# Kernel tuning notes

Hardware: AMD Instinct MI355X
Metric: run time of the kernel (lower is better)

Reference implementation:

```python
import jax, jax.numpy as jnp
import numpy as np

B, S, LQ = 32, 1024, 128
EMB = 256; H = 256; NH = 8; DH = H // NH
NCATE, NCONT, NNODE = 4, 8, 4
VOCAB = 50000
EPS = 1e-5
LK = S - LQ


def _ln(x, g, b):
    mu = jnp.mean(x, -1, keepdims=True)
    xc = x - mu
    var = jnp.mean(xc * xc, -1, keepdims=True)
    return xc * jax.lax.rsqrt(var + EPS) * g + b


def _leaky(x):
    return jnp.where(x >= 0, x, 0.01 * x)  # LeakyReLU slope 0.01 (torch default)


def setup_inputs() -> dict:
    key = jax.random.key(0)
    ks = jax.random.split(key, 48)
    rnd = lambda i, shape, scale=0.02: jax.random.normal(ks[i], shape, dtype=jnp.float32) * scale
    rng = np.random.default_rng(0)
    qidx = jnp.asarray(np.sort(rng.choice(S, LQ, replace=False)).astype(np.int64))
    cate_table = rnd(6, (VOCAB, EMB)).at[0].set(0.0)  # padding_idx=0
    inp = {
        "node": jax.random.normal(ks[0], (B, S, EMB * NNODE), dtype=jnp.float32),
        "cate": jax.random.randint(ks[1], (B, S, NCATE), 0, VOCAB),
        "cont": jax.random.normal(ks[2], (B, S, NCONT), dtype=jnp.float32),
        "query_index": qidx,
        "mask": jax.random.bernoulli(ks[3], 0.1, (B, LK)),
        "cate_table": cate_table,
        "pos_emb": rnd(4, (1, S, H)),
        "node_W": rnd(5, (EMB * NNODE, H)), "node_b": jnp.zeros((H,), jnp.float32),
        "node_ln_g": jnp.ones((H,), jnp.float32), "node_ln_b": jnp.zeros((H,), jnp.float32),
        "cate_W": rnd(7, (EMB * NCATE, H)), "cate_b": jnp.zeros((H,), jnp.float32),
        "cate_ln_g": jnp.ones((H,), jnp.float32), "cate_ln_b": jnp.zeros((H,), jnp.float32),
        "bn_g": jnp.ones((NCONT,), jnp.float32), "bn_b": jnp.zeros((NCONT,), jnp.float32),
        "cont_W": rnd(8, (NCONT, H)), "cont_b": jnp.zeros((H,), jnp.float32),
        "cont_ln_g": jnp.ones((H,), jnp.float32), "cont_ln_b": jnp.zeros((H,), jnp.float32),
        "comb_W": rnd(9, (3 * H, H)), "comb_b": jnp.zeros((H,), jnp.float32),
        "comb_ln_g": jnp.ones((H,), jnp.float32), "comb_ln_b": jnp.zeros((H,), jnp.float32),
        "q_W": rnd(10, (H, H)), "q_b": jnp.zeros((H,), jnp.float32),
        "k_W": rnd(11, (H, H)), "k_b": jnp.zeros((H,), jnp.float32),
        "v_W": rnd(12, (H, H)), "v_b": jnp.zeros((H,), jnp.float32),
        "reg_W1": rnd(13, (H, H)), "reg_b1": jnp.zeros((H,), jnp.float32),
        "reg_ln_g": jnp.ones((H,), jnp.float32), "reg_ln_b": jnp.zeros((H,), jnp.float32),
        "reg_W2": rnd(14, (H, H)), "reg_b2": jnp.zeros((H,), jnp.float32),
    }
    return inp


def reference(node, cate, cont, query_index, mask, cate_table, pos_emb,
              node_W, node_b, node_ln_g, node_ln_b,
              cate_W, cate_b, cate_ln_g, cate_ln_b,
              bn_g, bn_b, cont_W, cont_b, cont_ln_g, cont_ln_b,
              comb_W, comb_b, comb_ln_g, comb_ln_b,
              q_W, q_b, k_W, k_b, v_W, v_b,
              reg_W1, reg_b1, reg_ln_g, reg_ln_b, reg_W2, reg_b2):
    # --- three embedding branches: Linear -> LayerNorm ---
    node_e = _ln(node @ node_W + node_b, node_ln_g, node_ln_b)
    ce = cate_table[cate].reshape(B, S, NCATE * EMB)  # embedding gather
    cate_e = _ln(ce @ cate_W + cate_b, cate_ln_g, cate_ln_b)
    # BatchNorm1d (training-mode batch stats, biased var) over flattened [B*S, C]
    cf = cont.reshape(-1, NCONT)
    mu = jnp.mean(cf, 0)
    var = jnp.mean((cf - mu) ** 2, 0)
    cn = ((cf - mu) * jax.lax.rsqrt(var + EPS) * bn_g + bn_b).reshape(B, S, NCONT)
    cont_e = _ln(cn @ cont_W + cont_b, cont_ln_g, cont_ln_b)
    # --- combine + positions ---
    seq = jnp.concatenate([node_e, cate_e, cont_e], -1)       # [B,S,3H]
    seq = _ln(_leaky(seq) @ comb_W + comb_b, comb_ln_g, comb_ln_b) + pos_emb  # [B,S,H]
    # --- gather-split cross attention: queries vs complement keys ---
    is_q = jnp.zeros((S,), bool).at[query_index].set(True)
    key_index = jnp.nonzero(~is_q, size=LK)[0]                # setdiff1d, static size
    q = seq[:, query_index]                                   # [B,LQ,H]
    kv = seq[:, key_index]                                    # [B,LK,H]
    Q = (q @ q_W + q_b).reshape(B, LQ, NH, DH).transpose(0, 2, 1, 3)
    K = (kv @ k_W + k_b).reshape(B, LK, NH, DH).transpose(0, 2, 1, 3)
    V = (kv @ v_W + v_b).reshape(B, LK, NH, DH).transpose(0, 2, 1, 3)
    scale = jnp.float32(1.0 / np.sqrt(DH))
    scores = jnp.einsum('bhqd,bhkd->bhqk', Q, K) * scale      # [B,NH,LQ,LK]
    scores = jnp.where(mask[:, None, None, :], jnp.float32(-1e9), scores)
    attn = jax.nn.softmax(scores, -1)                         # dropout = identity (eval)
    out = jnp.einsum('bhqk,bhkd->bhqd', attn, V).transpose(0, 2, 1, 3).reshape(B, LQ, H)
    h = _leaky(_ln(out @ reg_W1 + reg_b1, reg_ln_g, reg_ln_b))
    return h @ reg_W2 + reg_b2                                # [B,LQ,H]
```

## Files before the change

### kernel.cpp

```cpp
#include <hip/hip_runtime.h>
#include <cstdint>

#define EPSV 1e-5f
#define AS1 __attribute__((address_space(1)))
#define AS3 __attribute__((address_space(3)))

#define VMCNT_BAR(N) do { \
    asm volatile("s_waitcnt vmcnt(" #N ") lgkmcnt(0)" ::: "memory"); \
    __builtin_amdgcn_sched_barrier(0); \
    __builtin_amdgcn_s_barrier(); } while (0)

typedef __attribute__((ext_vector_type(8))) short short8v;
typedef __attribute__((ext_vector_type(4))) float float4v;

__device__ inline unsigned short f2bf(float f) {
    union { float f; unsigned int u; } v; v.f = f;
    unsigned int r = v.u + 0x7FFF + ((v.u >> 16) & 1);
    return (unsigned short)(r >> 16);
}

__device__ inline size_t bidx(int n, int k) {
    return ((size_t)(k >> 5) << 13) + ((size_t)(n >> 4) << 9)
         + (((k >> 3) & 3) << 7) + ((n & 15) << 3) + (k & 7);
}

__device__ inline void gld16(const unsigned short* g, unsigned short* d) {
    __builtin_amdgcn_global_load_lds((const AS1 void*)g, (AS3 void*)d, 16, 0, 0);
}

__device__ inline void issue_b(const unsigned short* Bc, int s, unsigned short* bsb,
                               int w, int l) {
    const unsigned short* g = Bc + ((size_t)s << 13) + (w << 9) + (l << 3);
    unsigned short* d = bsb + (w << 9) + (l << 3);
    #pragma unroll
    for (int i = 0; i < 4; ++i)
        gld16(g + (i << 11), d + (i << 11));
}

__device__ inline void issue_b8(const unsigned short* Bc, int s, unsigned short* bsb,
                                int w, int l) {
    const unsigned short* g = Bc + ((size_t)(2 * s) << 13);
    #pragma unroll
    for (int i = 0; i < 4; ++i) {
        int blk = (w + i * 8) << 9;
        gld16(g + blk + (l << 3), bsb + blk + (l << 3));
    }
}

__global__ __launch_bounds__(256) void prep1_k(
    const float* __restrict__ contp, float* __restrict__ stats,
    const unsigned char* __restrict__ msrc, int* __restrict__ flags,
    const int* __restrict__ qidx, int* __restrict__ kmap,
    const float* __restrict__ nW, const float* __restrict__ cW, const float* __restrict__ mW,
    const float* __restrict__ qW, const float* __restrict__ kW, const float* __restrict__ vW,
    const float* __restrict__ r1W, const float* __restrict__ r2W,
    unsigned short* __restrict__ nO, unsigned short* __restrict__ cO, unsigned short* __restrict__ mO,
    unsigned short* __restrict__ qO, unsigned short* __restrict__ kO, unsigned short* __restrict__ vO,
    unsigned short* __restrict__ r1O, unsigned short* __restrict__ r2O)
{
    __shared__ float T[64][65];
    __shared__ float ss[8], sq[8];
    __shared__ int flag[1024];
    __shared__ int psc[256];
    const int bid = blockIdx.x;
    const int tid = threadIdx.x;

    if (bid < 256) {
        const float* W; unsigned short* O; int K, tile;
        if (bid < 64)       { W = nW; O = nO; K = 1024; tile = bid; }
        else if (bid < 128) { W = cW; O = cO; K = 1024; tile = bid - 64; }
        else if (bid < 176) { W = mW; O = mO; K = 768;  tile = bid - 128; }
        else {
            int s = (bid - 176) >> 4; tile = (bid - 176) & 15; K = 256;
            switch (s) {
                case 0: W = qW;  O = qO;  break;
                case 1: W = kW;  O = kO;  break;
                case 2: W = vW;  O = vO;  break;
                case 3: W = r1W; O = r1O; break;
                default: W = r2W; O = r2O; break;
            }
        }
        int kTiles = K >> 6;
        int k0 = (tile % kTiles) * 64, n0 = (tile / kTiles) * 64;
        int c = tid & 63, r4 = tid >> 6;
        #pragma unroll
        for (int rr = 0; rr < 64; rr += 4) {
            int r = rr + r4;
            T[r][c] = W[(size_t)(k0 + r) * 256 + n0 + c];
        }
        __syncthreads();
        #pragma unroll
        for (int rr = 0; rr < 64; rr += 4) {
            int n = rr + r4;
            O[bidx(n0 + n, k0 + c)] = f2bf(T[c][n]);
        }
    } else if (bid < 512) {
        if (tid < 8) { ss[tid] = 0.f; sq[tid] = 0.f; }
        __syncthreads();
        int gt = (bid - 256) * 256 + tid;
        float s = 0.f, q = 0.f;
        for (int e = gt; e < 32768*8; e += 256*256) { float v = contp[e]; s += v; q += v*v; }
        int f = gt & 7;
        atomicAdd(&ss[f], s);
        atomicAdd(&sq[f], q);
        __syncthreads();
        if (tid < 8) { atomicAdd(&stats[tid], ss[tid]); atomicAdd(&stats[8+tid], sq[tid]); }
    } else if (bid < 624) {
        int i = (bid - 512) * 256 + tid;
        unsigned char v = msrc[i];
        bool u8  = v && (i & 3);
        bool i32 = v && !(i & 3) && ((i & 7) == 4);
        unsigned long long bu = __ballot(u8);
        unsigned long long bi = __ballot(i32);
        if ((tid & 63) == 0) {
            if (bu) atomicOr(&flags[0], 1);
            if (bi) atomicOr(&flags[1], 1);
        }
    } else {
        #pragma unroll
        for (int j = 0; j < 4; ++j) flag[tid*4 + j] = 0;
        __syncthreads();
        if (tid < 128) flag[qidx[tid]] = 1;
        __syncthreads();
        int loc[4], cnt = 0;
        #pragma unroll
        for (int j = 0; j < 4; ++j) { loc[j] = 1 - flag[tid*4 + j]; cnt += loc[j]; }
        psc[tid] = cnt;
        __syncthreads();
        for (int off = 1; off < 256; off <<= 1) {
            int v = (tid >= off) ? psc[tid - off] : 0;
            __syncthreads();
            psc[tid] += v;
            __syncthreads();
        }
        int pos = psc[tid] - cnt;
        #pragma unroll
        for (int j = 0; j < 4; ++j)
            if (loc[j]) kmap[pos++] = tid*4 + j;
    }
}

__global__ __launch_bounds__(256) void prep2_k(
    const unsigned char* __restrict__ msrc, const int* __restrict__ flags,
    unsigned char* __restrict__ mu8,
    const int* __restrict__ qidx, const int* __restrict__ kmap,
    int* __restrict__ qmap, int* __restrict__ krmap,
    const float* __restrict__ contp, const float* __restrict__ stats,
    const float* __restrict__ bn_g, const float* __restrict__ bn_b,
    const float* __restrict__ W, const float* __restrict__ bias,
    const float* __restrict__ g, const float* __restrict__ bL,
    unsigned short* __restrict__ seq3)
{
    __shared__ float Ws[8][256];
    __shared__ float sscale[8], sshift[8];
    __shared__ float cr[8];
    __shared__ float red[8];
    const int bid = blockIdx.x, tid = threadIdx.x;

    if (bid < 112) {
        int i = bid * 256 + tid;
        int mode = flags[0] ? 0 : (flags[1] ? 1 : 2);
        unsigned char v;
        if (mode == 0)      v = msrc[i] ? 1 : 0;
        else if (mode == 1) v = ((const int*)msrc)[i] ? 1 : 0;
        else                v = ((const long long*)msrc)[i] ? 1 : 0;
        mu8[i] = v;
    } else if (bid < 224) {
        int i = (bid - 112) * 256 + tid;
        if (i < 32*128) { int b = i >> 7; int t2 = i & 127; qmap[i] = b*1024 + qidx[t2]; }
        if (i < 32*896) { int b = i / 896; int t2 = i - b*896; krmap[i] = b*1024 + kmap[t2]; }
    } else {
        #pragma unroll
        for (int d = 0; d < 8; ++d) Ws[d][tid] = W[d*256 + tid];
        if (tid < 8) {
            float mean = stats[tid] * (1.0f/32768.0f);
            float var  = stats[8+tid] * (1.0f/32768.0f) - mean*mean;
            float r = rsqrtf(var + EPSV);
            float sc = r * bn_g[tid];
            sscale[tid] = sc;
            sshift[tid] = bn_b[tid] - mean*sc;
        }
        __syncthreads();
        int lane = tid & 63, wv = tid >> 6;
        float gv = g[tid], bv = bL[tid], biasv = bias[tid];
        for (int row = bid - 224; row < 32768; row += 2048) {
            if (tid < 8) cr[tid] = contp[(size_t)row*8 + tid]*sscale[tid] + sshift[tid];
            __syncthreads();
            float acc = biasv;
            #pragma unroll
            for (int d = 0; d < 8; ++d) acc += cr[d]*Ws[d][tid];
            float s = acc;
            #pragma unroll
            for (int o = 32; o; o >>= 1) s += __shfl_xor(s, o);
            if (lane == 0) red[wv] = s;
            __syncthreads();
            float mu = (red[0]+red[1]+red[2]+red[3]) * (1.0f/256.0f);
            float dc = acc - mu;
            float qv = dc*dc;
            #pragma unroll
            for (int o = 32; o; o >>= 1) qv += __shfl_xor(qv, o);
            if (lane == 0) red[4+wv] = qv;
            __syncthreads();
            float var = (red[4]+red[5]+red[6]+red[7]) * (1.0f/256.0f);
            float y = dc * rsqrtf(var + EPSV) * gv + bv;
            y = (y >= 0.f) ? y : 0.01f*y;
            seq3[(size_t)row*768 + 512 + tid] = f2bf(y);
            __syncthreads();
        }
    }
}

__global__ __launch_bounds__(512, 4) void gemm_nc_k(
    const float* __restrict__ node, const int* __restrict__ cate,
    const float* __restrict__ table,
    const unsigned short* __restrict__ nWt, const unsigned short* __restrict__ cWt,
    const float* __restrict__ nb, const float* __restrict__ cb,
    const float* __restrict__ nlg, const float* __restrict__ nlb,
    const float* __restrict__ clg, const float* __restrict__ clb,
    unsigned short* __restrict__ Y)
{
    __shared__ union UN {
        unsigned short A[2][4096];
        struct { float S[64][4]; float Q[64][4]; } red;
    } U;
    __shared__ unsigned short Bs[2][16384];
    const int t = threadIdx.x;
    const bool isC = blockIdx.x >= 512;
    const int bm = (isC ? (int)blockIdx.x - 512 : (int)blockIdx.x) * 64;
    const int w = t >> 6, l = t & 63, lr = l & 15, lg = l >> 4;
    const int wm = w >> 2, wn = w & 3;
    const int ar = t >> 3;
    const int ac = (t & 7) * 8;
    const int aw = ((ac >> 5) << 11) + ((ar >> 4) << 9)
                 + (((ac >> 3) & 3) << 7) + ((ar & 15) << 3);

    const unsigned short* Bc = isC ? cWt : nWt;
    const float* bias = isC ? cb : nb;
    const float* lng  = isC ? clg : nlg;
    const float* lnbp = isC ? clb : nlb;
    const int colOff = isC ? 256 : 0;

    const float* apf = node + (size_t)(bm + ar) * 1024 + ac;
    int4 idx4 = {0,0,0,0};
    if (isC) idx4 = *(const int4*)&cate[(bm + ar) * 4];

    float4v acc[2][4];
    #pragma unroll
    for (int i = 0; i < 2; ++i)
        #pragma unroll
        for (int j = 0; j < 4; ++j) acc[i][j] = (float4v)0.f;

    float4 rA0, rA1;

    auto loadA = [&](int s) {
        const float* p;
        if (isC) {
            int kt = s * 64 + ac;
            int g = kt >> 8;
            int idx = (g == 0) ? idx4.x : (g == 1) ? idx4.y : (g == 2) ? idx4.z : idx4.w;
            p = table + (size_t)idx * 256 + (kt & 255);
        } else {
            p = apf + s * 64;
        }
        rA0 = *(const float4*)p;
        rA1 = *(const float4*)(p + 4);
    };
    auto writeA = [&](unsigned short* Ab) {
        short8v v;
        v[0] = (short)f2bf(rA0.x); v[1] = (short)f2bf(rA0.y);
        v[2] = (short)f2bf(rA0.z); v[3] = (short)f2bf(rA0.w);
        v[4] = (short)f2bf(rA1.x); v[5] = (short)f2bf(rA1.y);
        v[6] = (short)f2bf(rA1.z); v[7] = (short)f2bf(rA1.w);
        *(short8v*)&Ab[aw] = v;
    };
    auto comp = [&](const unsigned short* Ab, const unsigned short* bsb) {
        #pragma unroll
        for (int kk = 0; kk < 2; ++kk) {
            short8v af[2], bf[4];
            #pragma unroll
            for (int i = 0; i < 2; ++i)
                af[i] = *(const short8v*)&Ab[kk*2048 + ((wm*2 + i) << 9) + (lg << 7) + (lr << 3)];
            #pragma unroll
            for (int j = 0; j < 4; ++j)
                bf[j] = *(const short8v*)&bsb[kk*8192 + ((wn*4 + j) << 9) + (lg << 7) + (lr << 3)];
            #pragma unroll
            for (int i = 0; i < 2; ++i)
                #pragma unroll
                for (int j = 0; j < 4; ++j)
                    acc[i][j] = __builtin_amdgcn_mfma_f32_16x16x32_bf16(af[i], bf[j], acc[i][j], 0, 0, 0);
        }
    };

    issue_b8(Bc, 0, &Bs[0][0], w, l);
    loadA(0);
    writeA(U.A[0]);
    VMCNT_BAR(0);

    for (int s = 0; s < 16; ++s) {
        const int cur = s & 1;
        if (s + 1 < 16) {
            issue_b8(Bc, s + 1, &Bs[1 - cur][0], w, l);
            loadA(s + 1);
        }
        __builtin_amdgcn_sched_barrier(0);
        comp(U.A[cur], &Bs[cur][0]);
        if (s + 1 < 16) {
            writeA(U.A[1 - cur]);
            VMCNT_BAR(0);
        }
    }

    #pragma unroll
    for (int j = 0; j < 4; ++j) {
        float bvj = bias[wn*64 + j*16 + lr];
        #pragma unroll
        for (int i = 0; i < 2; ++i)
            #pragma unroll
            for (int r4 = 0; r4 < 4; ++r4) acc[i][j][r4] += bvj;
    }
    __syncthreads();
    #pragma unroll
    for (int i = 0; i < 2; ++i) {
        float ps[4], qs[4];
        #pragma unroll
        for (int r4 = 0; r4 < 4; ++r4) {
            float a0 = acc[i][0][r4], a1 = acc[i][1][r4],
                  a2 = acc[i][2][r4], a3 = acc[i][3][r4];
            ps[r4] = (a0 + a1) + (a2 + a3);
            qs[r4] = (a0*a0 + a1*a1) + (a2*a2 + a3*a3);
        }
        #pragma unroll
        for (int o = 1; o < 16; o <<= 1)
            #pragma unroll
            for (int r4 = 0; r4 < 4; ++r4) {
                ps[r4] += __shfl_xor(ps[r4], o);
                qs[r4] += __shfl_xor(qs[r4], o);
            }
        if (lr == 0) {
            #pragma unroll
            for (int r4 = 0; r4 < 4; ++r4) {
                int rlc = wm*32 + i*16 + lg*4 + r4;
                U.red.S[rlc][wn] = ps[r4];
                U.red.Q[rlc][wn] = qs[r4];
            }
        }
    }
    __syncthreads();
    #pragma unroll
    for (int i = 0; i < 2; ++i) {
        float mu[4], rstd[4];
        #pragma unroll
        for (int r4 = 0; r4 < 4; ++r4) {
            int rlc = wm*32 + i*16 + lg*4 + r4;
            float s  = (U.red.S[rlc][0] + U.red.S[rlc][1]) + (U.red.S[rlc][2] + U.red.S[rlc][3]);
            float qq = (U.red.Q[rlc][0] + U.red.Q[rlc][1]) + (U.red.Q[rlc][2] + U.red.Q[rlc][3]);
            float m_ = s * (1.0f/256.0f);
            mu[r4] = m_;
            rstd[r4] = rsqrtf(qq * (1.0f/256.0f) - m_*m_ + EPSV);
        }
        #pragma unroll
        for (int j = 0; j < 4; ++j) {
            int c = wn*64 + j*16 + lr;
            float gv = lng[c], b2 = lnbp[c];
            #pragma unroll
            for (int r4 = 0; r4 < 4; ++r4) {
                int row = bm + wm*32 + i*16 + lg*4 + r4;
                float y = (acc[i][j][r4] - mu[r4]) * rstd[r4] * gv + b2;
                y = (y >= 0.f) ? y : 0.01f*y;
                Y[(size_t)row * 768 + colOff + c] = f2bf(y);
            }
        }
    }
}

__global__ __launch_bounds__(512, 4) void gemm_comb_k(
    const unsigned short* __restrict__ A,
    const unsigned short* __restrict__ Bc,
    const float* __restrict__ bias,
    const float* __restrict__ lng, const float* __restrict__ lnbp,
    const float* __restrict__ pos,
    unsigned short* __restrict__ Y)
{
    __shared__ union UC {
        unsigned short A[2][4096];
        struct { float S[64][4]; float Q[64][4]; } red;
    } U;
    __shared__ unsigned short Bs[2][16384];
    const int t = threadIdx.x;
    const int bm = blockIdx.x * 64;
    const int w = t >> 6, l = t & 63, lr = l & 15, lg = l >> 4;
    const int wm = w >> 2, wn = w & 3;
    const int ar = t >> 3;
    const int ak = (t & 7) * 8;
    const int aw = ((ak >> 5) << 11) + ((ar >> 4) << 9)
                 + (((ak >> 3) & 3) << 7) + ((ar & 15) << 3);

    const unsigned short* ap = A + (size_t)(bm + ar) * 768 + ak;

    float4v acc[2][4];
    #pragma unroll
    for (int i = 0; i < 2; ++i)
        #pragma unroll
        for (int j = 0; j < 4; ++j) acc[i][j] = (float4v)0.f;

    short8v aA;

    auto comp = [&](const unsigned short* Ab, const unsigned short* bsb) {
        #pragma unroll
        for (int kk = 0; kk < 2; ++kk) {
            short8v af[2], bf[4];
            #pragma unroll
            for (int i = 0; i < 2; ++i)
                af[i] = *(const short8v*)&Ab[kk*2048 + ((wm*2 + i) << 9) + (lg << 7) + (lr << 3)];
            #pragma unroll
            for (int j = 0; j < 4; ++j)
                bf[j] = *(const short8v*)&bsb[kk*8192 + ((wn*4 + j) << 9) + (lg << 7) + (lr << 3)];
            #pragma unroll
            for (int i = 0; i < 2; ++i)
                #pragma unroll
                for (int j = 0; j < 4; ++j)
                    acc[i][j] = __builtin_amdgcn_mfma_f32_16x16x32_bf16(af[i], bf[j], acc[i][j], 0, 0, 0);
        }
    };

    issue_b8(Bc, 0, &Bs[0][0], w, l);
    aA = *(const short8v*)(ap);
    *(short8v*)&U.A[0][aw] = aA;
    VMCNT_BAR(0);

    for (int s = 0; s < 12; ++s) {
        const int cur = s & 1;
        if (s + 1 < 12) {
            issue_b8(Bc, s + 1, &Bs[1 - cur][0], w, l);
            aA = *(const short8v*)(ap + (s + 1) * 64);
        }
        __builtin_amdgcn_sched_barrier(0);
        comp(U.A[cur], &Bs[cur][0]);
        if (s + 1 < 12) {
            *(short8v*)&U.A[1 - cur][aw] = aA;
            VMCNT_BAR(0);
        }
    }

    #pragma unroll
    for (int j = 0; j < 4; ++j) {
        float bvj = bias[wn*64 + j*16 + lr];
        #pragma unroll
        for (int i = 0; i < 2; ++i)
            #pragma unroll
            for (int r4 = 0; r4 < 4; ++r4) acc[i][j][r4] += bvj;
    }
    __syncthreads();
    #pragma unroll
    for (int i = 0; i < 2; ++i) {
        float ps[4], qs[4];
        #pragma unroll
        for (int r4 = 0; r4 < 4; ++r4) {
            float a0 = acc[i][0][r4], a1 = acc[i][1][r4],
                  a2 = acc[i][2][r4], a3 = acc[i][3][r4];
            ps[r4] = (a0 + a1) + (a2 + a3);
            qs[r4] = (a0*a0 + a1*a1) + (a2*a2 + a3*a3);
        }
        #pragma unroll
        for (int o = 1; o < 16; o <<= 1)
            #pragma unroll
            for (int r4 = 0; r4 < 4; ++r4) {
                ps[r4] += __shfl_xor(ps[r4], o);
                qs[r4] += __shfl_xor(qs[r4], o);
            }
        if (lr == 0) {
            #pragma unroll
            for (int r4 = 0; r4 < 4; ++r4) {
                int rlc = wm*32 + i*16 + lg*4 + r4;
                U.red.S[rlc][wn] = ps[r4];
                U.red.Q[rlc][wn] = qs[r4];
            }
        }
    }
    __syncthreads();
    #pragma unroll
    for (int i = 0; i < 2; ++i) {
        float mu[4], rstd[4];
        #pragma unroll
        for (int r4 = 0; r4 < 4; ++r4) {
            int rlc = wm*32 + i*16 + lg*4 + r4;
            float s  = (U.red.S[rlc][0] + U.red.S[rlc][1]) + (U.red.S[rlc][2] + U.red.S[rlc][3]);
            float qq = (U.red.Q[rlc][0] + U.red.Q[rlc][1]) + (U.red.Q[rlc][2] + U.red.Q[rlc][3]);
            float m_ = s * (1.0f/256.0f);
            mu[r4] = m_;
            rstd[r4] = rsqrtf(qq * (1.0f/256.0f) - m_*m_ + EPSV);
        }
        #pragma unroll
        for (int j = 0; j < 4; ++j) {
            int c = wn*64 + j*16 + lr;
            float gv = lng[c], b2 = lnbp[c];
            #pragma unroll
            for (int r4 = 0; r4 < 4; ++r4) {
                int row = bm + wm*32 + i*16 + lg*4 + r4;
                float y = (acc[i][j][r4] - mu[r4]) * rstd[r4] * gv + b2
                        + pos[(size_t)(row & 1023) * 256 + c];
                Y[(size_t)row * 256 + c] = f2bf(y);
            }
        }
    }
}

__global__ __launch_bounds__(512, 4) void gemm_qkv_k(
    const unsigned short* __restrict__ seq,
    const int* __restrict__ qmap, const int* __restrict__ krmap,
    const unsigned short* __restrict__ qWt, const unsigned short* __restrict__ kWt,
    const unsigned short* __restrict__ vWt,
    const float* __restrict__ qb, const float* __restrict__ kb, const float* __restrict__ vb,
    unsigned short* __restrict__ Qo, unsigned short* __restrict__ Ko,
    unsigned short* __restrict__ Vt)
{
    __shared__ unsigned short Asl[2][4096];
    __shared__ unsigned short Bs[2][16384];
    const int t = threadIdx.x;
    const int bid = blockIdx.x;
    int seg, bm;
    const int* gmap; const unsigned short* Bc; const float* bias;
    if (bid < 64)       { seg = 0; bm = bid * 64;         gmap = qmap;  Bc = qWt; bias = qb; }
    else if (bid < 512) { seg = 1; bm = (bid - 64) * 64;  gmap = krmap; Bc = kWt; bias = kb; }
    else                { seg = 2; bm = (bid - 512) * 64; gmap = krmap; Bc = vWt; bias = vb; }
    const int w = t >> 6, l = t & 63, lr = l & 15, lg = l >> 4;
    const int wm = w >> 2, wn = w & 3;
    const int ar = t >> 3;
    const int ak = (t & 7) * 8;
    const int aw = ((ak >> 5) << 11) + ((ar >> 4) << 9)
                 + (((ak >> 3) & 3) << 7) + ((ar & 15) << 3);

    const unsigned short* ap = seq + (size_t)gmap[bm + ar] * 256 + ak;

    float4v acc[2][4];
    #pragma unroll
    for (int i = 0; i < 2; ++i)
        #pragma unroll
        for (int j = 0; j < 4; ++j) acc[i][j] = (float4v)0.f;

    short8v aA;

    auto comp = [&](const unsigned short* Ab, const unsigned short* bsb) {
        #pragma unroll
        for (int kk = 0; kk < 2; ++kk) {
            short8v af[2], bf[4];
            #pragma unroll
            for (int i = 0; i < 2; ++i)
                af[i] = *(const short8v*)&Ab[kk*2048 + ((wm*2 + i) << 9) + (lg << 7) + (lr << 3)];
            #pragma unroll
            for (int j = 0; j < 4; ++j)
                bf[j] = *(const short8v*)&bsb[kk*8192 + ((wn*4 + j) << 9) + (lg << 7) + (lr << 3)];
            #pragma unroll
            for (int i = 0; i < 2; ++i)
                #pragma unroll
                for (int j = 0; j < 4; ++j)
                    acc[i][j] = __builtin_amdgcn_mfma_f32_16x16x32_bf16(af[i], bf[j], acc[i][j], 0, 0, 0);
        }
    };

    issue_b8(Bc, 0, &Bs[0][0], w, l);
    aA = *(const short8v*)(ap);
    *(short8v*)&Asl[0][aw] = aA;
    VMCNT_BAR(0);

    for (int s = 0; s < 4; ++s) {
        const int cur = s & 1;
        if (s + 1 < 4) {
            issue_b8(Bc, s + 1, &Bs[1 - cur][0], w, l);
            aA = *(const short8v*)(ap + (s + 1) * 64);
        }
        __builtin_amdgcn_sched_barrier(0);
        comp(Asl[cur], &Bs[cur][0]);
        if (s + 1 < 4) {
            *(short8v*)&Asl[1 - cur][aw] = aA;
            VMCNT_BAR(0);
        }
    }

    unsigned short* outp = (seg == 0) ? Qo : (seg == 1) ? Ko : Vt;
    #pragma unroll
    for (int j = 0; j < 4; ++j) {
        int c = wn*64 + j*16 + lr;
        float bvj = bias[c];
        #pragma unroll
        for (int i = 0; i < 2; ++i) {
            #pragma unroll
            for (int r4 = 0; r4 < 4; ++r4) {
                int rl = wm*32 + i*16 + lg*4 + r4;
                float val = acc[i][j][r4] + bvj;
                if (seg < 2) {
                    outp[(size_t)(bm + rl) * 256 + c] = f2bf(val);
                } else {
                    int vbk = bm / 896;
                    int kl = bm - vbk * 896 + rl;
                    outp[((size_t)vbk * 256 + c) * 896 + kl] = f2bf(val);
                }
            }
        }
    }
}

template<int EPI>
__global__ __launch_bounds__(256) void gemm_reg_k(
    const unsigned short* __restrict__ Asrc,
    const unsigned short* __restrict__ Bc,
    const float* __restrict__ bias,
    const float* __restrict__ ln_g,
    const float* __restrict__ ln_b,
    void* __restrict__ Cout)
{
    __shared__ union UR {
        unsigned short A[2][4096];
        struct { float S[64][4]; float Q[64][4]; } red;
    } U;
    __shared__ unsigned short Bs[2][16384];
    const int t = threadIdx.x;
    const int bm = blockIdx.x * 64;
    const int w = t >> 6, l = t & 63, lr = l & 15, lg = l >> 4;
    const int ar = t >> 2;
    const int ac = (t & 3) * 16;
    const int aw0 = (((t & 3) >> 1) << 11) + ((ar >> 4) << 9)
                  + ((((t & 3) * 2) & 3) << 7) + ((ar & 15) << 3);
    const int aw1 = aw0 + 128;

    const unsigned short* ap = Asrc + (size_t)(bm + ar) * 256 + ac;

    float4v acc[4][4];
    #pragma unroll
    for (int i = 0; i < 4; ++i)
        #pragma unroll
        for (int j = 0; j < 4; ++j) acc[i][j] = (float4v)0.f;

    short8v a0A, a1A, a0B, a1B;

    auto comp = [&](const unsigned short* Ab, const unsigned short* bsb) {
        #pragma unroll
        for (int kk = 0; kk < 2; ++kk) {
            short8v af[4], bf[4];
            #pragma unroll
            for (int i = 0; i < 4; ++i)
                af[i] = *(const short8v*)&Ab[kk*2048 + i*512 + lg*128 + lr*8];
            #pragma unroll
            for (int j = 0; j < 4; ++j)
                bf[j] = *(const short8v*)&bsb[kk*8192 + ((w*4 + j) << 9) + (lg << 7) + (lr << 3)];
            #pragma unroll
            for (int i = 0; i < 4; ++i)
                #pragma unroll
                for (int j = 0; j < 4; ++j)
                    acc[i][j] = __builtin_amdgcn_mfma_f32_16x16x32_bf16(af[i], bf[j], acc[i][j], 0, 0, 0);
        }
    };

    issue_b(Bc, 0, &Bs[0][0], w, l);
    issue_b(Bc, 1, &Bs[0][8192], w, l);
    a0A = *(const short8v*)(ap);
    a1A = *(const short8v*)(ap + 8);
    for (int s = 0; s < 4; ++s) {
        int cur = s & 1;
        __syncthreads();
        *(short8v*)&U.A[cur][aw0] = a0A;
        *(short8v*)&U.A[cur][aw1] = a1A;
        __syncthreads();
        if (s + 1 < 4) {
            issue_b(Bc, 2*(s+1),     &Bs[1 - cur][0],    w, l);
            issue_b(Bc, 2*(s+1) + 1, &Bs[1 - cur][8192], w, l);
            a0B = *(const short8v*)(ap + (s + 1) * 64);
            a1B = *(const short8v*)(ap + (s + 1) * 64 + 8);
        }
        comp(U.A[cur], &Bs[cur][0]);
        a0A = a0B; a1A = a1B;
    }

    #pragma unroll
    for (int j = 0; j < 4; ++j) {
        float bvj = bias[w*64 + j*16 + lr];
        #pragma unroll
        for (int i = 0; i < 4; ++i)
            #pragma unroll
            for (int r4 = 0; r4 < 4; ++r4) acc[i][j][r4] += bvj;
    }

    if (EPI == 0) {
        #pragma unroll
        for (int i = 0; i < 4; ++i)
            #pragma unroll
            for (int j = 0; j < 4; ++j) {
                int c = w*64 + j*16 + lr;
                #pragma unroll
                for (int r4 = 0; r4 < 4; ++r4) {
                    int rl = i*16 + lg*4 + r4;
                    ((float*)Cout)[(size_t)(bm + rl) * 256 + c] = acc[i][j][r4];
                }
            }
    } else {
        __syncthreads();
        #pragma unroll
        for (int i = 0; i < 4; ++i) {
            float ps[4], qs[4];
            #pragma unroll
            for (int r4 = 0; r4 < 4; ++r4) {
                float a0 = acc[i][0][r4], a1 = acc[i][1][r4],
                      a2 = acc[i][2][r4], a3 = acc[i][3][r4];
                ps[r4] = (a0 + a1) + (a2 + a3);
                qs[r4] = (a0*a0 + a1*a1) + (a2*a2 + a3*a3);
            }
            #pragma unroll
            for (int o = 1; o < 16; o <<= 1)
                #pragma unroll
                for (int r4 = 0; r4 < 4; ++r4) {
                    ps[r4] += __shfl_xor(ps[r4], o);
                    qs[r4] += __shfl_xor(qs[r4], o);
                }
            if (lr == 0) {
                #pragma unroll
                for (int r4 = 0; r4 < 4; ++r4) {
                    U.red.S[i*16 + lg*4 + r4][w] = ps[r4];
                    U.red.Q[i*16 + lg*4 + r4][w] = qs[r4];
                }
            }
        }
        __syncthreads();
        #pragma unroll
        for (int i = 0; i < 4; ++i) {
            float mu[4], rstd[4];
            #pragma unroll
            for (int r4 = 0; r4 < 4; ++r4) {
                int rl = i*16 + lg*4 + r4;
                float s  = (U.red.S[rl][0] + U.red.S[rl][1]) + (U.red.S[rl][2] + U.red.S[rl][3]);
                float qq = (U.red.Q[rl][0] + U.red.Q[rl][1]) + (U.red.Q[rl][2] + U.red.Q[rl][3]);
                float m_ = s * (1.0f/256.0f);
                mu[r4] = m_;
                rstd[r4] = rsqrtf(qq * (1.0f/256.0f) - m_*m_ + EPSV);
            }
            #pragma unroll
            for (int j = 0; j < 4; ++j) {
                int c = w*64 + j*16 + lr;
                float gv = ln_g[c], b2 = ln_b[c];
                #pragma unroll
                for (int r4 = 0; r4 < 4; ++r4) {
                    int row = bm + i*16 + lg*4 + r4;
                    float y = (acc[i][j][r4] - mu[r4]) * rstd[r4] * gv + b2;
                    y = (y >= 0.f) ? y : 0.01f*y;
                    ((unsigned short*)Cout)[(size_t)row * 256 + c] = f2bf(y);
                }
            }
        }
    }
}

__global__ __launch_bounds__(256) void attn_mfma_k(
    const unsigned short* __restrict__ Qb,
    const unsigned short* __restrict__ Kb,
    const unsigned short* __restrict__ Vtb,
    const unsigned char* __restrict__ mask,
    unsigned short* __restrict__ out)
{
    __shared__ unsigned short Pw[4][16][72];
    const int t = threadIdx.x;
    const int w = t >> 6, l = t & 63;
    const int lr = l & 15, lg = l >> 4;
    const int bx = blockIdx.x;
    const int qh = bx & 1, h = (bx >> 1) & 7, b = bx >> 4;
    const int qrow0 = b*128 + qh*64 + w*16;

    short8v qf = *(const short8v*)&Qb[(size_t)(qrow0 + lr)*256 + h*32 + lg*8];

    const unsigned short* Kbase = Kb + (size_t)b*896*256 + h*32;
    const unsigned short* Vbase = Vtb + ((size_t)b*256 + h*32)*896;
    const unsigned char* mrow = mask + b*896;

    float4v O0 = (float4v)0.f, O1 = (float4v)0.f;
    float m[4], lsum[4];
    #pragma unroll
    for (int r = 0; r < 4; ++r) { m[r] = -3.0e38f; lsum[r] = 0.f; }

    short8v kf[4], vf[4];
    int mk[4];
    #pragma unroll
    for (int i = 0; i < 4; ++i) {
        kf[i] = *(const short8v*)&Kbase[(size_t)(i*16 + lr)*256 + lg*8];
        mk[i] = mrow[i*16 + lr];
    }
    #pragma unroll
    for (int kc = 0; kc < 2; ++kc)
        #pragma unroll
        for (int nt = 0; nt < 2; ++nt)
            vf[kc*2+nt] = *(const short8v*)&Vbase[(size_t)(nt*16 + lr)*896 + kc*32 + lg*8];

    for (int kt3 = 0; kt3 < 14; ++kt3) {
        const int kb2 = kt3*64 + 64;
        short8v kf2[4], vf2[4];
        int mk2[4];
        if (kt3 < 13) {
            #pragma unroll
            for (int i = 0; i < 4; ++i) {
                kf2[i] = *(const short8v*)&Kbase[(size_t)(kb2 + i*16 + lr)*256 + lg*8];
                mk2[i] = mrow[kb2 + i*16 + lr];
            }
            #pragma unroll
            for (int kc = 0; kc < 2; ++kc)
                #pragma unroll
                for (int nt = 0; nt < 2; ++nt)
                    vf2[kc*2+nt] = *(const short8v*)&Vbase[(size_t)(nt*16 + lr)*896 + kb2 + kc*32 + lg*8];
        }
        float4v s4[4];
        #pragma unroll
        for (int i = 0; i < 4; ++i)
            s4[i] = __builtin_amdgcn_mfma_f32_16x16x32_bf16(qf, kf[i], (float4v)0.f, 0, 0, 0);
        #pragma unroll
        for (int i = 0; i < 4; ++i)
            #pragma unroll
            for (int r = 0; r < 4; ++r)
                s4[i][r] = mk[i] ? -1e9f : s4[i][r] * 0.17677669529663687f;
        float tm[4];
        #pragma unroll
        for (int r = 0; r < 4; ++r)
            tm[r] = fmaxf(fmaxf(s4[0][r], s4[1][r]), fmaxf(s4[2][r], s4[3][r]));
        #pragma unroll
        for (int o = 1; o < 16; o <<= 1)
            #pragma unroll
            for (int r = 0; r < 4; ++r) tm[r] = fmaxf(tm[r], __shfl_xor(tm[r], o));
        float resc[4];
        #pragma unroll
        for (int r = 0; r < 4; ++r) {
            float mn = fmaxf(m[r], tm[r]);
            resc[r] = __expf(m[r] - mn);
            m[r] = mn;
        }
        float rs[4] = {0.f, 0.f, 0.f, 0.f};
        #pragma unroll
        for (int i = 0; i < 4; ++i)
            #pragma unroll
            for (int r = 0; r < 4; ++r) {
                float p = __expf(s4[i][r] - m[r]);
                s4[i][r] = p;
                rs[r] += p;
            }
        #pragma unroll
        for (int o = 1; o < 16; o <<= 1)
            #pragma unroll
            for (int r = 0; r < 4; ++r) rs[r] += __shfl_xor(rs[r], o);
        #pragma unroll
        for (int r = 0; r < 4; ++r) lsum[r] = lsum[r]*resc[r] + rs[r];
        #pragma unroll
        for (int r = 0; r < 4; ++r) { O0[r] *= resc[r]; O1[r] *= resc[r]; }
        #pragma unroll
        for (int i = 0; i < 4; ++i)
            #pragma unroll
            for (int r = 0; r < 4; ++r)
                Pw[w][lg*4 + r][i*16 + lr] = f2bf(s4[i][r]);
        #pragma unroll
        for (int kc = 0; kc < 2; ++kc) {
            short8v pf = *(const short8v*)&Pw[w][lr][kc*32 + lg*8];
            O0 = __builtin_amdgcn_mfma_f32_16x16x32_bf16(pf, vf[kc*2+0], O0, 0, 0, 0);
            O1 = __builtin_amdgcn_mfma_f32_16x16x32_bf16(pf, vf[kc*2+1], O1, 0, 0, 0);
        }
        if (kt3 < 13) {
            #pragma unroll
            for (int i = 0; i < 4; ++i) { kf[i] = kf2[i]; mk[i] = mk2[i]; vf[i] = vf2[i]; }
        }
    }
    #pragma unroll
    for (int r = 0; r < 4; ++r) {
        float inv = 1.0f / lsum[r];
        size_t row = (size_t)(qrow0 + lg*4 + r);
        out[row*256 + h*32 + lr]      = f2bf(O0[r] * inv);
        out[row*256 + h*32 + 16 + lr] = f2bf(O1[r] * inv);
    }
}

extern "C" void kernel_launch(void* const* d_in, const int* in_sizes, int n_in,
                              void* d_out, int out_size, void* d_ws, size_t ws_size,
                              hipStream_t stream)
{
    const float* node       = (const float*)d_in[0];
    const int*   cate       = (const int*)d_in[1];
    const float* cont       = (const float*)d_in[2];
    const int*   qidx       = (const int*)d_in[3];
    const unsigned char* mask = (const unsigned char*)d_in[4];
    const float* cate_table = (const float*)d_in[5];
    const float* pos_emb    = (const float*)d_in[6];
    const float* node_W     = (const float*)d_in[7];
    const float* node_b     = (const float*)d_in[8];
    const float* node_ln_g  = (const float*)d_in[9];
    const float* node_ln_b  = (const float*)d_in[10];
    const float* cate_W     = (const float*)d_in[11];
    const float* cate_b     = (const float*)d_in[12];
    const float* cate_ln_g  = (const float*)d_in[13];
    const float* cate_ln_b  = (const float*)d_in[14];
    const float* bn_g       = (const float*)d_in[15];
    const float* bn_b       = (const float*)d_in[16];
    const float* cont_W     = (const float*)d_in[17];
    const float* cont_b     = (const float*)d_in[18];
    const float* cont_ln_g  = (const float*)d_in[19];
    const float* cont_ln_b  = (const float*)d_in[20];
    const float* comb_W     = (const float*)d_in[21];
    const float* comb_b     = (const float*)d_in[22];
    const float* comb_ln_g  = (const float*)d_in[23];
    const float* comb_ln_b  = (const float*)d_in[24];
    const float* q_W        = (const float*)d_in[25];
    const float* q_b        = (const float*)d_in[26];
    const float* k_W        = (const float*)d_in[27];
    const float* k_b        = (const float*)d_in[28];
    const float* v_W        = (const float*)d_in[29];
    const float* v_b        = (const float*)d_in[30];
    const float* reg_W1     = (const float*)d_in[31];
    const float* reg_b1     = (const float*)d_in[32];
    const float* reg_ln_g   = (const float*)d_in[33];
    const float* reg_ln_b   = (const float*)d_in[34];
    const float* reg_W2     = (const float*)d_in[35];
    const float* reg_b2     = (const float*)d_in[36];

    char* ws = (char*)d_ws;
    unsigned short* seq3bf = (unsigned short*)(ws + 0);
    unsigned short* seqbf  = (unsigned short*)(ws + 83886080);
    unsigned short* Qbf    = (unsigned short*)(ws + 100663296);
    unsigned short* Kbf    = (unsigned short*)(ws + 102760448);
    unsigned short* Vtbf   = (unsigned short*)(ws + 117440512);
    unsigned short* AObf   = (unsigned short*)(ws + 132120576);
    unsigned short* Hbf    = (unsigned short*)(ws + 0);
    float* stats = (float*)(ws + 165675008);
    int*   flags = (int*)  (ws + 165675072);
    int*   kmap  = (int*)  (ws + 165675136);
    int*   qmap  = (int*)  (ws + 165678720);
    int*   krmap = (int*)  (ws + 165695104);
    unsigned char* mu8 = (unsigned char*)(ws + 165809792);
    unsigned short* node_Wt = (unsigned short*)(ws + 165838464);
    unsigned short* cate_Wt = (unsigned short*)(ws + 166362752);
    unsigned short* comb_Wt = (unsigned short*)(ws + 166887040);
    unsigned short* q_Wt    = (unsigned short*)(ws + 167280256);
    unsigned short* k_Wt    = (unsigned short*)(ws + 167411328);
    unsigned short* v_Wt    = (unsigned short*)(ws + 167542400);
    unsigned short* r1_Wt   = (unsigned short*)(ws + 167673472);
    unsigned short* r2_Wt   = (unsigned short*)(ws + 167804544);
    float* outp = (float*)d_out;

    hipMemsetAsync(stats, 0, 128, stream);
    prep1_k<<<625, 256, 0, stream>>>(cont, stats, mask, flags, qidx, kmap,
        node_W, cate_W, comb_W, q_W, k_W, v_W, reg_W1, reg_W2,
        node_Wt, cate_Wt, comb_Wt, q_Wt, k_Wt, v_Wt, r1_Wt, r2_Wt);
    prep2_k<<<2272, 256, 0, stream>>>(mask, flags, mu8, qidx, kmap, qmap, krmap,
        cont, stats, bn_g, bn_b, cont_W, cont_b, cont_ln_g, cont_ln_b, seq3bf);
    gemm_nc_k<<<1024, 512, 0, stream>>>(node, cate, cate_table, node_Wt, cate_Wt,
        node_b, cate_b, node_ln_g, node_ln_b, cate_ln_g, cate_ln_b, seq3bf);
    gemm_comb_k<<<512, 512, 0, stream>>>(seq3bf, comb_Wt, comb_b,
        comb_ln_g, comb_ln_b, pos_emb, seqbf);
    gemm_qkv_k<<<960, 512, 0, stream>>>(seqbf, qmap, krmap, q_Wt, k_Wt, v_Wt,
        q_b, k_b, v_b, Qbf, Kbf, Vtbf);
    attn_mfma_k<<<512, 256, 0, stream>>>(Qbf, Kbf, Vtbf, mu8, AObf);
    gemm_reg_k<3><<<64, 256, 0, stream>>>(AObf, r1_Wt, reg_b1, reg_ln_g, reg_ln_b, Hbf);
    gemm_reg_k<0><<<64, 256, 0, stream>>>(Hbf, r2_Wt, reg_b2, nullptr, nullptr, outp);
}
```

Measured before the change: 235.0 us.

## Triple-buffer comb and QKV GEMMs with direct global-to-LDS A loads

The combine and QKV projection GEMMs move from double to triple buffering, issuing loads two K-steps ahead and waiting with a partial vmcnt instead of draining all loads every step. The A tile now goes straight from global memory into LDS through gld16 with a remapped thread-to-element layout, so it no longer passes through registers and a separate LDS store. More shared memory per block forces the launch bounds down from 4 to 2 blocks per CU, trading occupancy for deeper prefetch.

```diff
diff --git a/kernel.cpp b/kernel.cpp
--- a/kernel.cpp
+++ b/kernel.cpp
@@ -373,7 +373,7 @@
     }
 }
 
-__global__ __launch_bounds__(512, 4) void gemm_comb_k(
+__global__ __launch_bounds__(512, 2) void gemm_comb_k(
     const unsigned short* __restrict__ A,
     const unsigned short* __restrict__ Bc,
     const float* __restrict__ bias,
@@ -382,20 +382,18 @@
     unsigned short* __restrict__ Y)
 {
     __shared__ union UC {
-        unsigned short A[2][4096];
+        unsigned short A[3][4096];
         struct { float S[64][4]; float Q[64][4]; } red;
     } U;
-    __shared__ unsigned short Bs[2][16384];
+    __shared__ unsigned short Bs[3][16384];
     const int t = threadIdx.x;
     const int bm = blockIdx.x * 64;
     const int w = t >> 6, l = t & 63, lr = l & 15, lg = l >> 4;
     const int wm = w >> 2, wn = w & 3;
-    const int ar = t >> 3;
-    const int ak = (t & 7) * 8;
-    const int aw = ((ak >> 5) << 11) + ((ar >> 4) << 9)
-                 + (((ak >> 3) & 3) << 7) + ((ar & 15) << 3);
-
-    const unsigned short* ap = A + (size_t)(bm + ar) * 768 + ak;
+    const int grow = ((t >> 2) & 0x30) | (t & 15);
+    const int gk   = ((t >> 3) & 0x20) | ((t >> 1) & 0x18);
+
+    const unsigned short* ap = A + (size_t)(bm + grow) * 768 + gk;
 
     float4v acc[2][4];
     #pragma unroll
@@ -403,8 +401,9 @@
         #pragma unroll
         for (int j = 0; j < 4; ++j) acc[i][j] = (float4v)0.f;
 
-    short8v aA;
-
+    auto issue_a = [&](int s, int buf) {
+        gld16(ap + s * 64, &U.A[buf][t << 3]);
+    };
     auto comp = [&](const unsigned short* Ab, const unsigned short* bsb) {
         #pragma unroll
         for (int kk = 0; kk < 2; ++kk) {
@@ -424,21 +423,23 @@
     };
 
     issue_b8(Bc, 0, &Bs[0][0], w, l);
-    aA = *(const short8v*)(ap);
-    *(short8v*)&U.A[0][aw] = aA;
-    VMCNT_BAR(0);
+    issue_a(0, 0);
+    issue_b8(Bc, 1, &Bs[1][0], w, l);
+    issue_a(1, 1);
+    VMCNT_BAR(5);
 
     for (int s = 0; s < 12; ++s) {
-        const int cur = s & 1;
-        if (s + 1 < 12) {
-            issue_b8(Bc, s + 1, &Bs[1 - cur][0], w, l);
-            aA = *(const short8v*)(ap + (s + 1) * 64);
+        const int cur = s % 3;
+        if (s + 2 < 12) {
+            const int nb = (s + 2) % 3;
+            issue_b8(Bc, s + 2, &Bs[nb][0], w, l);
+            issue_a(s + 2, nb);
         }
         __builtin_amdgcn_sched_barrier(0);
         comp(U.A[cur], &Bs[cur][0]);
         if (s + 1 < 12) {
-            *(short8v*)&U.A[1 - cur][aw] = aA;
-            VMCNT_BAR(0);
+            if (s + 2 < 12) VMCNT_BAR(5);
+            else            VMCNT_BAR(0);
         }
     }
 
@@ -505,7 +506,7 @@
     }
 }
 
-__global__ __launch_bounds__(512, 4) void gemm_qkv_k(
+__global__ __launch_bounds__(512, 2) void gemm_qkv_k(
     const unsigned short* __restrict__ seq,
     const int* __restrict__ qmap, const int* __restrict__ krmap,
     const unsigned short* __restrict__ qWt, const unsigned short* __restrict__ kWt,
@@ -514,8 +515,8 @@
     unsigned short* __restrict__ Qo, unsigned short* __restrict__ Ko,
     unsigned short* __restrict__ Vt)
 {
-    __shared__ unsigned short Asl[2][4096];
-    __shared__ unsigned short Bs[2][16384];
+    __shared__ unsigned short Asl[3][4096];
+    __shared__ unsigned short Bs[3][16384];
     const int t = threadIdx.x;
     const int bid = blockIdx.x;
     int seg, bm;
@@ -525,12 +526,10 @@
     else                { seg = 2; bm = (bid - 512) * 64; gmap = krmap; Bc = vWt; bias = vb; }
     const int w = t >> 6, l = t & 63, lr = l & 15, lg = l >> 4;
     const int wm = w >> 2, wn = w & 3;
-    const int ar = t >> 3;
-    const int ak = (t & 7) * 8;
-    const int aw = ((ak >> 5) << 11) + ((ar >> 4) << 9)
-                 + (((ak >> 3) & 3) << 7) + ((ar & 15) << 3);
-
-    const unsigned short* ap = seq + (size_t)gmap[bm + ar] * 256 + ak;
+    const int grow = ((t >> 2) & 0x30) | (t & 15);
+    const int gk   = ((t >> 3) & 0x20) | ((t >> 1) & 0x18);
+
+    const unsigned short* ap = seq + (size_t)gmap[bm + grow] * 256 + gk;
 
     float4v acc[2][4];
     #pragma unroll
@@ -538,8 +537,9 @@
         #pragma unroll
         for (int j = 0; j < 4; ++j) acc[i][j] = (float4v)0.f;
 
-    short8v aA;
-
+    auto issue_a = [&](int s, int buf) {
+        gld16(ap + s * 64, &Asl[buf][t << 3]);
+    };
     auto comp = [&](const unsigned short* Ab, const unsigned short* bsb) {
         #pragma unroll
         for (int kk = 0; kk < 2; ++kk) {
@@ -559,21 +559,23 @@
     };
 
     issue_b8(Bc, 0, &Bs[0][0], w, l);
-    aA = *(const short8v*)(ap);
-    *(short8v*)&Asl[0][aw] = aA;
-    VMCNT_BAR(0);
+    issue_a(0, 0);
+    issue_b8(Bc, 1, &Bs[1][0], w, l);
+    issue_a(1, 1);
+    VMCNT_BAR(5);
 
     for (int s = 0; s < 4; ++s) {
-        const int cur = s & 1;
-        if (s + 1 < 4) {
-            issue_b8(Bc, s + 1, &Bs[1 - cur][0], w, l);
-            aA = *(const short8v*)(ap + (s + 1) * 64);
+        const int cur = s % 3;
+        if (s + 2 < 4) {
+            const int nb = (s + 2) % 3;
+            issue_b8(Bc, s + 2, &Bs[nb][0], w, l);
+            issue_a(s + 2, nb);
         }
         __builtin_amdgcn_sched_barrier(0);
         comp(Asl[cur], &Bs[cur][0]);
         if (s + 1 < 4) {
-            *(short8v*)&Asl[1 - cur][aw] = aA;
-            VMCNT_BAR(0);
+            if (s + 2 < 4) VMCNT_BAR(5);
+            else           VMCNT_BAR(0);
         }
     }
 
```

Measured after the change: 245.9 us. 4.6% more time.
